# Kernel optimization log

Hardware: AMD Instinct MI355X
Metric: run time of the kernel (lower is better)

The kernel has to match this reference:

```python
import jax, jax.numpy as jnp
import numpy as np

_SQRT1_2 = 0.7071067811865476

B, S, D, N, NCH = 4, 2048, 1024, 32768, 8


def setup_inputs() -> dict:
    key = jax.random.key(0)
    ks = jax.random.split(key, 6)
    return {
        "x": jax.random.normal(ks[0], (B, S, D), jnp.float32),
        "h": jax.random.normal(ks[1], (B, S, D), jnp.float32),
        "emb": jax.random.normal(ks[2], (N, D), jnp.float32),
        "tau_offset": jax.random.normal(ks[3], (B, S, 1), jnp.float32),
        "w_read": jax.random.normal(ks[4], (N, D), jnp.float32),
        "w_write": jax.random.normal(ks[5], (N, D), jnp.float32),
        "n_chunks": NCH,
    }


def _srw_chunked(x, h, emb_unit, tau_offset, w_read, w_write, n_chunks):
    b, s, d = x.shape
    n = emb_unit.shape[0]
    cs = n // n_chunks
    h_bf = h.astype(jnp.bfloat16)
    x_bf = x.astype(jnp.bfloat16)
    emb_bf = emb_unit.astype(jnp.bfloat16)
    read_bf = w_read.astype(jnp.bfloat16)
    write_bf = w_write.astype(jnp.bfloat16)
    z1 = jnp.zeros((b, s, 1), jnp.float32)

    # ---- pass 1: online score statistics over chunks of N ----
    @jax.checkpoint
    def stats_step(carry, i):
        s_sum, sq_sum, cube_sum, ns_sum, ns_sq = carry
        ec = jax.lax.dynamic_slice_in_dim(emb_bf, i * cs, cs, axis=0)
        sc = (h_bf @ ec.T).astype(jnp.float32)  # [B,S,cs]
        s_sum = s_sum + sc.sum(-1, keepdims=True)
        sq_sum = sq_sum + (sc ** 2).sum(-1, keepdims=True)
        cube_sum = cube_sum + (sc ** 3).sum(-1, keepdims=True)
        pns = sc.mean(axis=(0, 1))  # per-neuron mean score [cs]
        return ((s_sum, sq_sum, cube_sum, ns_sum + pns.sum(), ns_sq + (pns ** 2).sum()), None)

    (s_sum, sq_sum, cube_sum, ns_sum, ns_sq), _ = jax.lax.scan(
        stats_step, (z1, z1, z1, jnp.float32(0.0), jnp.float32(0.0)), jnp.arange(n_chunks))

    s_mean = s_sum / n
    s_std = jnp.sqrt(sq_sum / n - s_mean ** 2) + 1e-08
    tau = s_mean + tau_offset * s_std
    cube_mean = cube_sum / n
    central_third = cube_mean - 3.0 * s_mean * s_std ** 2 - s_mean ** 3
    score_skew = jax.lax.stop_gradient((central_third / (s_std ** 3 + 1e-08)).mean())
    mean_score = ns_sum / n
    var_score = ns_sq / n - mean_score ** 2
    score_lb = var_score / (mean_score ** 2 + var_score + 0.01)

    # ---- pass 2: erf-threshold gate + read/write GEMM accumulate ----
    @jax.checkpoint
    def gate_step(carry, i):
        out, wcost, gmax, act, strong, phib, zsum, z075c, z030c, glg = carry
        s0 = i * cs
        ec = jax.lax.dynamic_slice_in_dim(emb_bf, s0, cs, axis=0)
        rc = jax.lax.dynamic_slice_in_dim(read_bf, s0, cs, axis=0)
        wc = jax.lax.dynamic_slice_in_dim(write_bf, s0, cs, axis=0)
        rc = rc / (jnp.linalg.norm(rc, axis=-1, keepdims=True) + 1e-08)
        wc = wc / (jnp.linalg.norm(wc, axis=-1, keepdims=True) + 1e-08)
        z = ((h_bf @ ec.T).astype(jnp.float32) - tau) / s_std  # [B,S,cs]
        phi = 0.5 * (1.0 + jax.lax.erf(z * _SQRT1_2))
        gate = jnp.where(z > 0, z * phi, 0.0)
        xr = x_bf @ rc.T  # [B,S,cs]
        c_out = ((gate.astype(jnp.bfloat16) * xr) @ wc).astype(jnp.float32)  # [B,S,D]
        g_safe = gate + 1e-08
        new = (
            out + c_out,
            wcost + gate.sum(-1, keepdims=True),
            jnp.maximum(gmax, gate.max(-1, keepdims=True)),
            act + (gate > 0.0).astype(jnp.float32).sum(-1, keepdims=True),
            strong + (gate > 0.5).astype(jnp.float32).sum(-1, keepdims=True),
            phib + ((phi > 0.95) | (phi < 0.05)).astype(jnp.float32).sum(-1, keepdims=True),
            zsum + jnp.where(z > 0, z, 0.0).sum(-1, keepdims=True),
            z075c + ((z > 0) & (z < 0.75)).astype(jnp.float32).sum(-1, keepdims=True),
            z030c + ((z > 0) & (z < 0.3)).astype(jnp.float32).sum(-1, keepdims=True),
            glg + (gate * jnp.log(g_safe)).sum(-1, keepdims=True),
        )
        return (new, None)

    init = (jnp.zeros((b, s, d), jnp.float32), z1, jnp.full((b, s, 1), -1e9, jnp.float32),
            z1, z1, z1, z1, z1, z1, z1)
    (raw_out, wcost, gmax, act, strong, phib, zsum, z075c, z030c, glg), _ = jax.lax.scan(
        gate_step, init, jnp.arange(n_chunks))

    den = jnp.maximum(wcost, 1.0)
    out = (raw_out / den).astype(jnp.bfloat16)
    score_std_out = s_std.mean()
    es_out = wcost.mean()
    active_n_mean = act.mean()
    z_mean_active = zsum / (act + 1e-08)
    active_eps = act + 1e-08
    z_lt_075_frac = jax.lax.stop_gradient((z075c / active_eps).mean())
    z_lt_030_frac = jax.lax.stop_gradient((z030c / active_eps).mean())
    tau_abs_mean = jax.lax.stop_gradient(tau).mean()
    active_per_token_std = jax.lax.stop_gradient(act).std()
    gate_sum_eps = wcost + 1e-08
    entropy_per_token = -glg / gate_sum_eps + jnp.log(gate_sum_eps)
    gate_entropy = jax.lax.stop_gradient(entropy_per_token).mean()
    return (out.astype(jnp.float32), act / n, gmax, score_lb, score_std_out, es_out,
            active_n_mean, strong / n, phib / n, z_mean_active, tau_abs_mean,
            z_lt_075_frac, z_lt_030_frac, score_skew, active_per_token_std, gate_entropy)


def reference(x, h, emb, tau_offset, w_read, w_write, n_chunks):
    emb_unit = emb / (jnp.linalg.norm(emb, axis=-1, keepdims=True) + 1e-08)
    return _srw_chunked(x, h, emb_unit, tau_offset, w_read, w_write, n_chunks)
```

## Files before the change

kernel.cpp:

```cpp
#include <hip/hip_runtime.h>

#define DEV __device__ __forceinline__

typedef __attribute__((ext_vector_type(4))) float f32x4;
typedef __attribute__((ext_vector_type(8))) short s16x8;
typedef __attribute__((ext_vector_type(8))) unsigned short u16x8;

static const int NTOK = 8192;
static const int DD   = 1024;
static const int NNEU = 32768;
static const int NC   = 8192;
static const int NREP = 8;

static const int OUT_ACT    = 8388608;
static const int OUT_GMAX   = 8396800;
static const int OUT_SLB    = 8404992;
static const int OUT_SSTD   = 8404993;
static const int OUT_ES     = 8404994;
static const int OUT_ANM    = 8404995;
static const int OUT_STRONG = 8404996;
static const int OUT_PHIB   = 8413188;
static const int OUT_ZMEAN  = 8421380;
static const int OUT_TAUM   = 8429572;
static const int OUT_Z75    = 8429573;
static const int OUT_Z30    = 8429574;
static const int OUT_SKEW   = 8429575;
static const int OUT_ASTD   = 8429576;
static const int OUT_ENT    = 8429577;

DEV unsigned short f2bf(float f){
  unsigned u = __float_as_uint(f);
  u += 0x7fffu + ((u >> 16) & 1u);
  return (unsigned short)(u >> 16);
}
DEV float bf2f(unsigned short h){ return __uint_as_float(((unsigned)h) << 16); }
DEV float rnd_bf(float f){ return bf2f(f2bf(f)); }

template<int AUX>
DEV void gl_lds16(const void* g, void* l){
  __builtin_amdgcn_global_load_lds(
      (const __attribute__((address_space(1))) unsigned int*)g,
      (__attribute__((address_space(3))) unsigned int*)l, 16, 0, AUX);
}

DEV f32x4 mfma16(s16x8 a, s16x8 b, f32x4 c){
  return __builtin_amdgcn_mfma_f32_16x16x32_bf16(a, b, c, 0, 0, 0);
}

template<int AUX>
DEV void stage4(const unsigned short* __restrict__ G, size_t ld, int k0,
                unsigned short* L, int t){
  #pragma unroll
  for (int i = 0; i < 4; i++){
    int ch = i*256 + t;
    int row = ch >> 3, c = ch & 7;
    int cs = c ^ (row & 7);
    int wb = (i*256 + (t & 192)) * 16;
    gl_lds16<AUX>(G + (size_t)row * ld + k0 + cs*8, (char*)L + wb);
  }
}

DEV void stageS(const unsigned short* __restrict__ S0, size_t ldS,
                unsigned short* L, int t){
  #pragma unroll
  for (int i = 0; i < 8; i++){
    int ch = i*256 + t;
    int row = ch >> 4, c = ch & 15;
    int cs = c ^ (row & 15);
    int wb = (i*256 + (t & 192)) * 16;
    gl_lds16<0>(S0 + (size_t)row * ldS + cs*8, (char*)L + wb);
  }
}

DEV s16x8 frg(const unsigned short* L, int R, int kk, int lq){
  int cc = ((kk >> 3) + lq) ^ (R & 7);
  return *(const s16x8*)((const char*)L + R*128 + cc*16);
}

DEV void waitv_bar(){
  asm volatile("s_waitcnt vmcnt(0)" ::: "memory");
  __builtin_amdgcn_s_barrier();
  __builtin_amdgcn_sched_barrier(0);
}

DEV int2 xcd64(){
  int orig = blockIdx.y * 64 + blockIdx.x;
  int xcd = orig & 7, p = orig >> 3;
  int sqy = p >> 6, off = p & 63;
  int2 r;
  r.x = xcd*8 + (off & 7);
  r.y = sqy*8 + (off >> 3);
  return r;
}


template<int RND, int PNS>
__global__ __launch_bounds__(256) void k_rncast(const float* __restrict__ in,
    unsigned short* __restrict__ o, const float* __restrict__ hs,
    float* __restrict__ ns){
  __shared__ float hsh[1024];
  __shared__ float pr[8];
  int t = threadIdx.x, l = t & 63, wv = t >> 6;
  if (PNS){
    for (int i = t; i < 1024; i += 256) hsh[i] = hs[i];
    __syncthreads();
  }
  int row = blockIdx.x * 4 + wv;
  const float4* rp = (const float4*)(in + (size_t)row * DD);
  float4 v[4];
  float ss = 0.f;
  #pragma unroll
  for (int j = 0; j < 4; j++){
    float4 a = rp[j*64 + l];
    if (RND){ a.x = rnd_bf(a.x); a.y = rnd_bf(a.y); a.z = rnd_bf(a.z); a.w = rnd_bf(a.w); }
    v[j] = a;
    ss += a.x*a.x + a.y*a.y + a.z*a.z + a.w*a.w;
  }
  #pragma unroll
  for (int d = 1; d < 64; d <<= 1) ss += __shfl_xor(ss, d);
  float inv = 1.f / (sqrtf(ss) + 1e-8f);
  float dot = 0.f;
  ushort4* op = (ushort4*)(o + (size_t)row * DD);
  #pragma unroll
  for (int j = 0; j < 4; j++){
    ushort4 r;
    r.x = f2bf(v[j].x * inv); r.y = f2bf(v[j].y * inv);
    r.z = f2bf(v[j].z * inv); r.w = f2bf(v[j].w * inv);
    op[j*64 + l] = r;
    if (PNS){
      int c0 = (j*64 + l)*4;
      dot += hsh[c0]*bf2f(r.x) + hsh[c0+1]*bf2f(r.y)
           + hsh[c0+2]*bf2f(r.z) + hsh[c0+3]*bf2f(r.w);
    }
  }
  if (PNS){
    #pragma unroll
    for (int d = 1; d < 64; d <<= 1) dot += __shfl_xor(dot, d);
    if (l == 0){
      float pns = dot * (1.f / 8192.f);
      pr[wv*2] = pns; pr[wv*2 + 1] = pns*pns;
    }
    __syncthreads();
    if (t == 0){
      atomicAdd(ns + 0, pr[0] + pr[2] + pr[4] + pr[6]);
      atomicAdd(ns + 1, pr[1] + pr[3] + pr[5] + pr[7]);
    }
  }
}

__global__ __launch_bounds__(256) void k_wnorm(const float* __restrict__ w_,
                                               float* __restrict__ inv_w){
  int t = threadIdx.x, l = t & 63, wv = t >> 6;
  int row = blockIdx.x * 4 + wv;
  const float4* wp = (const float4*)(w_ + (size_t)row * DD);
  float sw = 0.f;
  #pragma unroll
  for (int j = 0; j < 4; j++){
    float4 c = wp[j*64 + l];
    float c0 = rnd_bf(c.x), c1 = rnd_bf(c.y), c2 = rnd_bf(c.z), c3 = rnd_bf(c.w);
    sw += c0*c0 + c1*c1 + c2*c2 + c3*c3;
  }
  #pragma unroll
  for (int d = 1; d < 64; d <<= 1) sw += __shfl_xor(sw, d);
  if (l == 0) inv_w[row] = 1.f / (sqrtf(sw) + 1e-8f);
}

__global__ __launch_bounds__(256) void k_cast(const float* __restrict__ in,
                                              unsigned short* __restrict__ o){
  size_t i = (size_t)blockIdx.x * 256 + threadIdx.x;
  float4 v = ((const float4*)in)[i];
  ushort4 r;
  r.x = f2bf(v.x); r.y = f2bf(v.y); r.z = f2bf(v.z); r.w = f2bf(v.w);
  ((ushort4*)o)[i] = r;
}

__global__ __launch_bounds__(256) void k_wcnT(const float* __restrict__ w_,
    const float* __restrict__ invw, unsigned short* __restrict__ o){
  __shared__ unsigned short tile[64][65];
  int t = threadIdx.x;
  int n0b = blockIdx.x * 64, d0 = blockIdx.y * 64;
  #pragma unroll
  for (int i = 0; i < 16; i++){
    int idx = t + i*256;
    int r = idx >> 6, c = idx & 63;
    float v = w_[(size_t)(n0b + r) * DD + d0 + c];
    tile[c][r] = f2bf(rnd_bf(v) * invw[n0b + r]);
  }
  __syncthreads();
  #pragma unroll
  for (int i = 0; i < 16; i++){
    int idx = t + i*256;
    int rd = idx >> 6, cn = idx & 63;
    o[(size_t)(d0 + rd) * NNEU + n0b + cn] = tile[rd][cn];
  }
}

__global__ __launch_bounds__(256) void k_hsum(const unsigned short* __restrict__ hb,
                                              float* __restrict__ hs){
  int t = threadIdx.x; int r0 = blockIdx.x * 128;
  float s[4] = {0.f, 0.f, 0.f, 0.f};
  for (int r = 0; r < 128; r++){
    const unsigned short* row = hb + (size_t)(r0 + r) * DD;
    #pragma unroll
    for (int j = 0; j < 4; j++) s[j] += bf2f(row[j*256 + t]);
  }
  #pragma unroll
  for (int j = 0; j < 4; j++) atomicAdd(hs + j*256 + t, s[j]);
}


template<bool DO_STATS>
__global__ __launch_bounds__(256, 2) void k_score(
    const unsigned short* __restrict__ A, const unsigned short* __restrict__ Bm,
    float* __restrict__ s_sum, float* __restrict__ sq_sum, float* __restrict__ cu_sum,
    unsigned short* __restrict__ Sout, int do_store)
{
  __shared__ unsigned short lds[32768];
  const int t = threadIdx.x, l = t & 63, wv = t >> 6;
  const int wm = wv >> 1, wn = wv & 1;
  const int lq = l >> 4, lr = l & 15;
  int2 rm = xcd64();
  const int bx = rm.x, by = rm.y;
  const unsigned short* Ab = A  + (size_t)by * 128 * DD;
  const unsigned short* Bb = Bm + (size_t)bx * 128 * DD;
  f32x4 acc[4][4];
  #pragma unroll
  for (int m = 0; m < 4; m++)
    #pragma unroll
    for (int n = 0; n < 4; n++) acc[m][n] = (f32x4){0.f, 0.f, 0.f, 0.f};

  stage4<0>(Ab, DD, 0, lds, t);
  stage4<0>(Bb, DD, 0, lds + 8192, t);
  waitv_bar();
  int cur = 0;
  for (int ks = 0; ks < 16; ++ks){
    unsigned short* Lc = lds + cur*16384;
    if (ks + 1 < 16){
      unsigned short* Ln = lds + (cur^1)*16384;
      int k0 = (ks+1)*64;
      stage4<0>(Ab, DD, k0, Ln, t);
      stage4<0>(Bb, DD, k0, Ln + 8192, t);
    }
    #pragma unroll
    for (int kk = 0; kk < 64; kk += 32){
      s16x8 af[4], bf4[4];
      #pragma unroll
      for (int m = 0; m < 4; m++) af[m]  = frg(Lc, wm*64 + m*16 + lr, kk, lq);
      #pragma unroll
      for (int n = 0; n < 4; n++) bf4[n] = frg(Lc + 8192, wn*64 + n*16 + lr, kk, lq);
      #pragma unroll
      for (int m = 0; m < 4; m++)
        #pragma unroll
        for (int n = 0; n < 4; n++)
          acc[m][n] = mfma16(af[m], bf4[n], acc[m][n]);
    }
    waitv_bar();
    cur ^= 1;
  }

  unsigned short* sl = lds;
  #pragma unroll
  for (int m = 0; m < 4; m++)
  #pragma unroll
  for (int n = 0; n < 4; n++)
  #pragma unroll
  for (int r = 0; r < 4; r++){
    int rl = wm*64 + m*16 + lq*4 + r;
    int cl = wn*64 + n*16 + lr;
    sl[rl*136 + cl] = f2bf(acc[m][n][r]);
  }
  __syncthreads();

  int row = t >> 1, half = t & 1;
  const unsigned short* sp = &sl[row*136 + half*64];
  unsigned short* Sdst = Sout + (size_t)(by*128 + row) * NC + bx*128 + half*64;
  float s1 = 0.f, s2 = 0.f, s3 = 0.f;
  #pragma unroll
  for (int j = 0; j < 8; j++){
    u16x8 v = *(const u16x8*)(sp + j*8);
    if (do_store) *(u16x8*)(Sdst + j*8) = v;
    if (DO_STATS){
      #pragma unroll
      for (int e = 0; e < 8; e++){
        float f = bf2f(v[e]);
        s1 += f; float f2 = f*f; s2 += f2; s3 += f2*f;
      }
    }
  }
  if (DO_STATS){
    s1 += __shfl_xor(s1, 1); s2 += __shfl_xor(s2, 1); s3 += __shfl_xor(s3, 1);
    if (half == 0){
      int gr = by*128 + row;
      int rep = (bx & 7) * NTOK;
      atomicAdd(s_sum + rep + gr, s1);
      atomicAdd(sq_sum + rep + gr, s2);
      atomicAdd(cu_sum + rep + gr, s3);
    }
  }
}

__global__ __launch_bounds__(256) void k_tau(const float* __restrict__ s_sum,
    const float* __restrict__ sq_sum, const float* __restrict__ tof,
    float* __restrict__ tau, float* __restrict__ rstd){
  int i = blockIdx.x * 256 + threadIdx.x;
  float ssum = 0.f, sqsum = 0.f;
  #pragma unroll
  for (int k = 0; k < NREP; k++){
    ssum  += s_sum[k*NTOK + i];
    sqsum += sq_sum[k*NTOK + i];
  }
  float mean = ssum * (1.f / 32768.f);
  float var  = sqsum * (1.f / 32768.f) - mean*mean;
  float sstd = sqrtf(fmaxf(var, 0.f)) + 1e-8f;
  tau[i]  = mean + tof[i] * sstd;
  rstd[i] = 1.f / sstd;
}


__global__ __launch_bounds__(256, 2) void k_gateS(
    const unsigned short* __restrict__ Xb, const unsigned short* __restrict__ Rb,
    const float* __restrict__ tau, const float* __restrict__ rstd,
    unsigned short* __restrict__ SP, int n0,
    float* __restrict__ wcostp, float* __restrict__ gmaxp, float* __restrict__ actp,
    float* __restrict__ strongp, float* __restrict__ phibp, float* __restrict__ zsump,
    float* __restrict__ z075p, float* __restrict__ z030p, float* __restrict__ glgp)
{
  __shared__ unsigned short lds[32768];
  const int t = threadIdx.x, l = t & 63, wv = t >> 6;
  const int wm = wv >> 1, wn = wv & 1;
  const int lq = l >> 4, lr = l & 15;
  int2 rm = xcd64();
  const int bx = rm.x, by = rm.y;
  const unsigned short* Xp = Xb + (size_t)by * 128 * DD;
  const unsigned short* Rp = Rb + (size_t)(n0 + bx*128) * DD;
  const unsigned short* Stile = SP + (size_t)(by*128) * NC + bx*128;
  f32x4 accX[4][4];
  #pragma unroll
  for (int m = 0; m < 4; m++)
    #pragma unroll
    for (int n = 0; n < 4; n++) accX[m][n] = (f32x4){0.f,0.f,0.f,0.f};

  stage4<0>(Xp, DD, 0, lds, t);
  stage4<0>(Rp, DD, 0, lds + 8192, t);
  waitv_bar();
  int cur = 0;
  for (int ks = 0; ks < 16; ++ks){
    unsigned short* Lc = lds + cur*16384;
    if (ks + 1 < 16){
      unsigned short* Ln = lds + (cur^1)*16384;
      int k0 = (ks+1)*64;
      stage4<0>(Xp, DD, k0, Ln, t);
      stage4<0>(Rp, DD, k0, Ln + 8192, t);
    } else {
      stageS(Stile, NC, lds, t);
    }
    #pragma unroll
    for (int kk = 0; kk < 64; kk += 32){
      s16x8 af[4], bf4[4];
      #pragma unroll
      for (int m = 0; m < 4; m++) af[m]  = frg(Lc, wm*64 + m*16 + lr, kk, lq);
      #pragma unroll
      for (int n = 0; n < 4; n++) bf4[n] = frg(Lc + 8192, wn*64 + n*16 + lr, kk, lq);
      #pragma unroll
      for (int m = 0; m < 4; m++)
        #pragma unroll
        for (int n = 0; n < 4; n++)
          accX[m][n] = mfma16(af[m], bf4[n], accX[m][n]);
    }
    waitv_bar();
    cur ^= 1;
  }
  unsigned short* xrl = lds + 16384;
  #pragma unroll
  for (int m = 0; m < 4; m++)
  #pragma unroll
  for (int n = 0; n < 4; n++)
  #pragma unroll
  for (int r = 0; r < 4; r++){
    int rl = wm*64 + m*16 + lq*4 + r;
    int cl = wn*64 + n*16 + lr;
    int cs = (cl >> 3) ^ (rl & 15);
    xrl[rl*128 + cs*8 + (cl & 7)] = f2bf(accX[m][n][r]);
  }
  __syncthreads();

  int row = t >> 1, half = t & 1;
  int gr = by*128 + row;
  float tauv = tau[gr], rs = rstd[gr];
  unsigned short* Prow = SP + (size_t)gr * NC + bx*128 + half*64;
  float wsum = 0.f, gmx = 0.f, ac = 0.f, stc = 0.f, pb = 0.f;
  float zs = 0.f, z7 = 0.f, z3 = 0.f, gl = 0.f;
  #pragma unroll
  for (int jj = 0; jj < 8; jj++){
    int g  = half*8 + jj;
    int cs = g ^ (row & 15);
    u16x8 s8 = *(const u16x8*)&lds[row*128 + cs*8];
    u16x8 x8 = *(const u16x8*)&lds[16384 + row*128 + cs*8];
    u16x8 pv;
    #pragma unroll
    for (int e = 0; e < 8; e++){
      float sc = bf2f(s8[e]);
      float xr = bf2f(x8[e]);
      float z = (sc - tauv) * rs;
      float phi = 0.5f * (1.0f + erff(z * 0.70710678118654752440f));
      float gate = (z > 0.f) ? z * phi : 0.f;
      wsum += gate; gmx = fmaxf(gmx, gate);
      if (gate > 0.5f) stc += 1.f;
      if (fabsf(z) > 1.6448536f) pb += 1.f;
      if (z > 0.f){ ac += 1.f; zs += z; if (z < 0.75f) z7 += 1.f; if (z < 0.3f) z3 += 1.f; }
      gl += gate * __logf(gate + 1e-8f);
      pv[e] = f2bf(rnd_bf(gate) * xr);
    }
    *(u16x8*)(Prow + jj*8) = pv;
  }
  wsum += __shfl_xor(wsum, 1); gmx = fmaxf(gmx, __shfl_xor(gmx, 1));
  ac   += __shfl_xor(ac, 1);   stc += __shfl_xor(stc, 1);
  pb   += __shfl_xor(pb, 1);   zs  += __shfl_xor(zs, 1);
  z7   += __shfl_xor(z7, 1);   z3  += __shfl_xor(z3, 1);
  gl   += __shfl_xor(gl, 1);
  if (half == 0){
    int rep = (bx & 7) * NTOK;
    atomicAdd(wcostp + rep + gr, wsum);
    atomicMax((int*)(gmaxp + rep + gr), __float_as_int(gmx));
    atomicAdd(actp + rep + gr, ac);
    atomicAdd(strongp + rep + gr, stc);
    atomicAdd(phibp + rep + gr, pb);
    atomicAdd(zsump + rep + gr, zs);
    atomicAdd(z075p + rep + gr, z7);
    atomicAdd(z030p + rep + gr, z3);
    atomicAdd(glgp + rep + gr, gl);
  }
}

__global__ __launch_bounds__(256) void k_redw(const float* __restrict__ wcostp,
                                              float* __restrict__ wc){
  int i = blockIdx.x * 256 + threadIdx.x;
  float s = 0.f;
  #pragma unroll
  for (int k = 0; k < NREP; k++) s += wcostp[k*NTOK + i];
  wc[i] = s;
}


__global__ __launch_bounds__(256, 2) void k_out_gemm(
    const unsigned short* __restrict__ Pm, const unsigned short* __restrict__ Bt,
    float* __restrict__ outp, const float* __restrict__ wcost, int accum, int fin)
{
  __shared__ unsigned short lds[32768];
  const int t = threadIdx.x, l = t & 63, wv = t >> 6;
  const int wm = wv >> 1, wn = wv & 1;
  const int lq = l >> 4, lr = l & 15;
  const int bx = blockIdx.x, by = blockIdx.y;
  const unsigned short* Ab = Pm + (size_t)by * 128 * NC;
  const unsigned short* Bb = Bt + (size_t)bx * 128 * NNEU;
  f32x4 acc[4][4];
  #pragma unroll
  for (int m = 0; m < 4; m++)
    #pragma unroll
    for (int n = 0; n < 4; n++) acc[m][n] = (f32x4){0.f,0.f,0.f,0.f};

  const int NT = NC / 64;
  stage4<2>(Ab, NC, 0, lds, t);
  stage4<0>(Bb, NNEU, 0, lds + 8192, t);
  waitv_bar();
  int cur = 0;
  for (int ks = 0; ks < NT; ++ks){
    unsigned short* Lc = lds + cur*16384;
    if (ks + 1 < NT){
      unsigned short* Ln = lds + (cur^1)*16384;
      int k0 = (ks+1)*64;
      stage4<2>(Ab, NC, k0, Ln, t);
      stage4<0>(Bb, NNEU, k0, Ln + 8192, t);
    }
    #pragma unroll
    for (int kk = 0; kk < 64; kk += 32){
      s16x8 af[4], bf4[4];
      #pragma unroll
      for (int m = 0; m < 4; m++) af[m]  = frg(Lc, wm*64 + m*16 + lr, kk, lq);
      #pragma unroll
      for (int n = 0; n < 4; n++) bf4[n] = frg(Lc + 8192, wn*64 + n*16 + lr, kk, lq);
      #pragma unroll
      for (int m = 0; m < 4; m++)
        #pragma unroll
        for (int n = 0; n < 4; n++)
          acc[m][n] = mfma16(af[m], bf4[n], acc[m][n]);
    }
    waitv_bar();
    cur ^= 1;
  }
  #pragma unroll
  for (int m = 0; m < 4; m++)
  #pragma unroll
  for (int r = 0; r < 4; r++){
    int gr = by*128 + wm*64 + m*16 + lq*4 + r;
    float den = fin ? fmaxf(wcost[gr], 1.f) : 1.f;
    #pragma unroll
    for (int n = 0; n < 4; n++){
      int dc = bx*128 + wn*64 + n*16 + lr;
      float* o = outp + (size_t)gr * DD + dc;
      float v = acc[m][n][r];
      if (accum) v += *o;
      if (fin)   v = rnd_bf(v / den);
      *o = v;
    }
  }
}


__global__ __launch_bounds__(1024) void k_final(
    const float* __restrict__ s_sum, const float* __restrict__ sq_sum,
    const float* __restrict__ cu_sum, const float* __restrict__ tof,
    const float* __restrict__ wcostp, const float* __restrict__ gmaxp,
    const float* __restrict__ actp, const float* __restrict__ strongp,
    const float* __restrict__ phibp, const float* __restrict__ zsump,
    const float* __restrict__ z075p, const float* __restrict__ z030p,
    const float* __restrict__ glgp, const float* __restrict__ ns,
    float* __restrict__ out)
{
  int tid = threadIdx.x;
  float s0=0,s1=0,s2=0,s3=0,s4=0,s5=0,s6=0,s7=0,s8=0;
  for (int i = tid; i < NTOK; i += 1024){
    float ssum=0, sqsum=0, cusum=0, wc=0, gmax=0, ac=0, stc=0, pb=0, zsv=0, z7=0, z3=0, glv=0;
    #pragma unroll
    for (int k = 0; k < NREP; k++){
      int o = k*NTOK + i;
      ssum += s_sum[o]; sqsum += sq_sum[o]; cusum += cu_sum[o];
      wc += wcostp[o]; gmax = fmaxf(gmax, gmaxp[o]);
      ac += actp[o]; stc += strongp[o]; pb += phibp[o];
      zsv += zsump[o]; z7 += z075p[o]; z3 += z030p[o]; glv += glgp[o];
    }
    float mean = ssum * (1.f / 32768.f);
    float var  = sqsum * (1.f / 32768.f) - mean*mean;
    float sstd = sqrtf(fmaxf(var, 0.f)) + 1e-8f;
    float tauv = mean + tof[i] * sstd;
    out[OUT_ACT + i]    = ac * (1.f / 32768.f);
    out[OUT_GMAX + i]   = gmax;
    out[OUT_STRONG + i] = stc * (1.f / 32768.f);
    out[OUT_PHIB + i]   = pb * (1.f / 32768.f);
    out[OUT_ZMEAN + i]  = zsv / (ac + 1e-8f);
    float c3 = cusum * (1.f / 32768.f) - 3.f*mean*sstd*sstd - mean*mean*mean;
    float skew = c3 / (sstd*sstd*sstd + 1e-8f);
    float gse = wc + 1e-8f;
    float ent = -glv / gse + logf(gse);
    s0 += sstd; s1 += wc; s2 += ac; s3 += ac*ac; s4 += tauv;
    s5 += z7 / (ac + 1e-8f); s6 += z3 / (ac + 1e-8f); s7 += skew; s8 += ent;
  }
  __shared__ float rb[16][9];
  int lane = tid & 63, wid = tid >> 6;
  #pragma unroll
  for (int d = 1; d < 64; d <<= 1){
    s0 += __shfl_xor(s0,d); s1 += __shfl_xor(s1,d); s2 += __shfl_xor(s2,d);
    s3 += __shfl_xor(s3,d); s4 += __shfl_xor(s4,d); s5 += __shfl_xor(s5,d);
    s6 += __shfl_xor(s6,d); s7 += __shfl_xor(s7,d); s8 += __shfl_xor(s8,d);
  }
  if (lane == 0){
    rb[wid][0]=s0; rb[wid][1]=s1; rb[wid][2]=s2; rb[wid][3]=s3; rb[wid][4]=s4;
    rb[wid][5]=s5; rb[wid][6]=s6; rb[wid][7]=s7; rb[wid][8]=s8;
  }
  __syncthreads();
  if (tid == 0){
    float S[9];
    for (int k = 0; k < 9; k++){ float a = 0.f; for (int w2 = 0; w2 < 16; w2++) a += rb[w2][k]; S[k] = a; }
    const float inv = 1.f / 8192.f;
    float act_mean = S[2] * inv;
    out[OUT_SSTD] = S[0] * inv;
    out[OUT_ES]   = S[1] * inv;
    out[OUT_ANM]  = act_mean;
    out[OUT_ASTD] = sqrtf(fmaxf(S[3]*inv - act_mean*act_mean, 0.f));
    out[OUT_TAUM] = S[4] * inv;
    out[OUT_Z75]  = S[5] * inv;
    out[OUT_Z30]  = S[6] * inv;
    out[OUT_SKEW] = S[7] * inv;
    out[OUT_ENT]  = S[8] * inv;
    float ms = ns[0] * (1.f / 32768.f);
    float vs = ns[1] * (1.f / 32768.f) - ms*ms;
    out[OUT_SLB] = vs / (ms*ms + vs + 0.01f);
  }
}


extern "C" void kernel_launch(void* const* d_in, const int* in_sizes, int n_in,
                              void* d_out, int out_size, void* d_ws, size_t ws_size,
                              hipStream_t stream)
{
  (void)in_sizes; (void)n_in; (void)out_size;
  const float* x   = (const float*)d_in[0];
  const float* h   = (const float*)d_in[1];
  const float* emb = (const float*)d_in[2];
  const float* tof = (const float*)d_in[3];
  const float* wr  = (const float*)d_in[4];
  const float* ww  = (const float*)d_in[5];
  float* out = (float*)d_out;
  char* ws = (char*)d_ws;

  size_t off = 0;
  auto get = [&](size_t n){ size_t o = off; off += (n + 255) & ~(size_t)255; return o; };
  unsigned short* rcn_bf = (unsigned short*)(ws + get((size_t)NNEU*DD*2));
  unsigned short* emb_bf = (unsigned short*)(ws + get((size_t)NNEU*DD*2));
  unsigned short* wcnT   = (unsigned short*)(ws + get((size_t)DD*NNEU*2));
  unsigned short* h_bf   = (unsigned short*)(ws + get((size_t)NTOK*DD*2));
  unsigned short* x_bf   = (unsigned short*)(ws + get((size_t)NTOK*DD*2));
  float* inv_w   = (float*)(ws + get(NNEU*4));
  float* tau     = (float*)(ws + get(NTOK*4));
  float* rstd    = (float*)(ws + get(NTOK*4));
  float* wc_comb = (float*)(ws + get(NTOK*4));
  size_t zoff = off;
  float* hsum   = (float*)(ws + get(DD*4));
  float* s_sum  = (float*)(ws + get(NREP*NTOK*4));
  float* sq_sum = (float*)(ws + get(NREP*NTOK*4));
  float* cu_sum = (float*)(ws + get(NREP*NTOK*4));
  float* wcost  = (float*)(ws + get(NREP*NTOK*4));
  float* gmax   = (float*)(ws + get(NREP*NTOK*4));
  float* act    = (float*)(ws + get(NREP*NTOK*4));
  float* strong = (float*)(ws + get(NREP*NTOK*4));
  float* phib   = (float*)(ws + get(NREP*NTOK*4));
  float* zsum   = (float*)(ws + get(NREP*NTOK*4));
  float* z075   = (float*)(ws + get(NREP*NTOK*4));
  float* z030   = (float*)(ws + get(NREP*NTOK*4));
  float* glg    = (float*)(ws + get(NREP*NTOK*4));
  float* ns     = (float*)(ws + get(256));
  size_t zlen = off - zoff;

  const size_t szS = (size_t)NTOK * NC * 2;
  size_t poff = (off + 4095) & ~(size_t)4095;
  size_t avail = ws_size > poff ? ws_size - poff : 0;
  int kst = (int)(avail / szS);
  if (kst > 4) kst = 4;
  if (kst < 1) kst = 1;
  unsigned short* Sb = (unsigned short*)(ws + poff);

  hipMemsetAsync(ws + zoff, 0, zlen, stream);

  dim3 b256(256);
  dim3 gC(64, 64);
  k_cast<<<dim3(NTOK*DD/4/256), b256, 0, stream>>>(h, h_bf);
  k_cast<<<dim3(NTOK*DD/4/256), b256, 0, stream>>>(x, x_bf);
  k_hsum<<<dim3(NTOK/128), b256, 0, stream>>>(h_bf, hsum);
  k_rncast<0,1><<<dim3(NNEU/4), b256, 0, stream>>>(emb, emb_bf, hsum, ns);
  k_rncast<1,0><<<dim3(NNEU/4), b256, 0, stream>>>(wr, rcn_bf, nullptr, nullptr);
  k_wnorm<<<dim3(NNEU/4), b256, 0, stream>>>(ww, inv_w);

  for (int c = 0; c < 4; ++c){
    unsigned short* slot = Sb + (size_t)(c < kst ? c : 0) * NTOK * NC;
    k_score<true><<<gC, b256, 0, stream>>>(h_bf, emb_bf + (size_t)c*NC*DD,
        s_sum, sq_sum, cu_sum, slot, c < kst ? 1 : 0);
  }
  k_tau<<<dim3(NTOK/256), b256, 0, stream>>>(s_sum, sq_sum, tof, tau, rstd);
  k_wcnT<<<dim3(NNEU/64, DD/64), b256, 0, stream>>>(ww, inv_w, wcnT);

  for (int c = 0; c < 4; ++c){
    int slot_i = (c < kst) ? c : (c % kst);
    unsigned short* slot = Sb + (size_t)slot_i * NTOK * NC;
    if (c >= kst){
      k_score<false><<<gC, b256, 0, stream>>>(h_bf, emb_bf + (size_t)c*NC*DD,
          nullptr, nullptr, nullptr, slot, 1);
    }
    k_gateS<<<gC, b256, 0, stream>>>(x_bf, rcn_bf, tau, rstd, slot, c*NC,
        wcost, gmax, act, strong, phib, zsum, z075, z030, glg);
    if (c == 3) k_redw<<<dim3(NTOK/256), b256, 0, stream>>>(wcost, wc_comb);
    k_out_gemm<<<dim3(DD/128, NTOK/128), b256, 0, stream>>>(slot, wcnT + (size_t)c*NC,
        out, wc_comb, c > 0 ? 1 : 0, c == 3 ? 1 : 0);
  }
  k_final<<<dim3(1), dim3(1024), 0, stream>>>(s_sum, sq_sum, cu_sum, tof, wcost, gmax,
      act, strong, phib, zsum, z075, z030, glg, ns, out);
}
```

Baseline: 3.907 ms.

## Enlarge score and gate GEMM tiles to 256x256 with a 4-stage pipeline

The score and gate GEMM kernels move from 128x128 tiles with 256 threads and double-buffered BK=64 staging to 256x256 tiles with 512 threads. Staging becomes a 4-deep ring of BK=32 buffers with counted vmcnt waits, and s_setprio wraps the MFMA bursts. The gate kernel now reads the stored score tile straight from global memory into registers instead of staging it through LDS. The aim is more reuse per loaded byte and better latency hiding. The cost is 128KB of LDS per block, which likely allows only one block per CU, plus higher register pressure.

```diff
diff --git a/kernel.cpp b/kernel.cpp
--- a/kernel.cpp
+++ b/kernel.cpp
@@ -59,37 +59,41 @@
     gl_lds16<AUX>(G + (size_t)row * ld + k0 + cs*8, (char*)L + wb);
   }
 }
-
-DEV void stageS(const unsigned short* __restrict__ S0, size_t ldS,
-                unsigned short* L, int t){
-  #pragma unroll
-  for (int i = 0; i < 8; i++){
-    int ch = i*256 + t;
-    int row = ch >> 4, c = ch & 15;
-    int cs = c ^ (row & 15);
-    int wb = (i*256 + (t & 192)) * 16;
-    gl_lds16<0>(S0 + (size_t)row * ldS + cs*8, (char*)L + wb);
-  }
-}
-
 DEV s16x8 frg(const unsigned short* L, int R, int kk, int lq){
   int cc = ((kk >> 3) + lq) ^ (R & 7);
   return *(const s16x8*)((const char*)L + R*128 + cc*16);
 }
-
 DEV void waitv_bar(){
   asm volatile("s_waitcnt vmcnt(0)" ::: "memory");
   __builtin_amdgcn_s_barrier();
   __builtin_amdgcn_sched_barrier(0);
 }
 
-DEV int2 xcd64(){
-  int orig = blockIdx.y * 64 + blockIdx.x;
+DEV void stageK(const unsigned short* __restrict__ GA,
+                const unsigned short* __restrict__ GB,
+                int kt, unsigned short* Lb, int t){
+  #pragma unroll
+  for (int i = 0; i < 2; i++){
+    int ch = i*512 + t, row = ch >> 2, c = ch & 3;
+    gl_lds16<0>(GA + (size_t)row * DD + kt*32 + (c ^ (row & 3))*8,
+                (char*)Lb + (i*512 + (t & 448))*16);
+  }
+  #pragma unroll
+  for (int i = 0; i < 2; i++){
+    int ch = i*512 + t, row = ch >> 2, c = ch & 3;
+    gl_lds16<0>(GB + (size_t)row * DD + kt*32 + (c ^ (row & 3))*8,
+                (char*)Lb + 16384 + (i*512 + (t & 448))*16);
+  }
+}
+DEV s16x8 frg32(const unsigned short* L, int R, int lq){
+  int cs = lq ^ (R & 3);
+  return *(const s16x8*)(L + R*32 + cs*8);
+}
+
+DEV int2 xcd32(){
+  int orig = blockIdx.y * 32 + blockIdx.x;
   int xcd = orig & 7, p = orig >> 3;
-  int sqy = p >> 6, off = p & 63;
-  int2 r;
-  r.x = xcd*8 + (off & 7);
-  r.y = sqy*8 + (off >> 3);
+  int2 r; r.x = xcd*4 + (p & 3); r.y = p >> 2;
   return r;
 }
 
@@ -209,75 +213,85 @@
 }
 
 
+#define CORE_LOOP(GA, GB)                                                     \
+  stageK(GA, GB, 0, lds + 0*16384, t);                                        \
+  stageK(GA, GB, 1, lds + 1*16384, t);                                        \
+  stageK(GA, GB, 2, lds + 2*16384, t);                                        \
+  _Pragma("unroll 1")                                                         \
+  for (int ks = 0; ks < 32; ++ks){                                            \
+    if (ks < 30)       asm volatile("s_waitcnt vmcnt(8)" ::: "memory");       \
+    else if (ks == 30) asm volatile("s_waitcnt vmcnt(4)" ::: "memory");       \
+    else               asm volatile("s_waitcnt vmcnt(0)" ::: "memory");       \
+    __builtin_amdgcn_s_barrier();                                             \
+    __builtin_amdgcn_sched_barrier(0);                                        \
+    if (ks + 3 < 32) stageK(GA, GB, ks + 3, lds + ((ks+3)&3)*16384, t);       \
+    const unsigned short* lA = lds + (ks&3)*16384;                            \
+    const unsigned short* lB = lA + 8192;                                     \
+    s16x8 af[8], b0, b1;                                                      \
+    _Pragma("unroll")                                                         \
+    for (int m = 0; m < 8; m++) af[m] = frg32(lA, wm*128 + m*16 + lr, lq);    \
+    b0 = frg32(lB, wn*64 +  0 + lr, lq);                                      \
+    b1 = frg32(lB, wn*64 + 16 + lr, lq);                                      \
+    __builtin_amdgcn_s_setprio(1);                                            \
+    _Pragma("unroll")                                                         \
+    for (int m = 0; m < 8; m++) acc[m][0] = mfma16(af[m], b0, acc[m][0]);     \
+    _Pragma("unroll")                                                         \
+    for (int m = 0; m < 8; m++) acc[m][1] = mfma16(af[m], b1, acc[m][1]);     \
+    __builtin_amdgcn_s_setprio(0);                                            \
+    b0 = frg32(lB, wn*64 + 32 + lr, lq);                                      \
+    b1 = frg32(lB, wn*64 + 48 + lr, lq);                                      \
+    __builtin_amdgcn_s_setprio(1);                                            \
+    _Pragma("unroll")                                                         \
+    for (int m = 0; m < 8; m++) acc[m][2] = mfma16(af[m], b0, acc[m][2]);     \
+    _Pragma("unroll")                                                         \
+    for (int m = 0; m < 8; m++) acc[m][3] = mfma16(af[m], b1, acc[m][3]);     \
+    __builtin_amdgcn_s_setprio(0);                                            \
+  }                                                                           \
+  __syncthreads();
+
+
 template<bool DO_STATS>
-__global__ __launch_bounds__(256, 2) void k_score(
+__global__ __launch_bounds__(512, 2) void k_score(
     const unsigned short* __restrict__ A, const unsigned short* __restrict__ Bm,
     float* __restrict__ s_sum, float* __restrict__ sq_sum, float* __restrict__ cu_sum,
     unsigned short* __restrict__ Sout, int do_store)
 {
-  __shared__ unsigned short lds[32768];
+  __shared__ unsigned short lds[65536];
   const int t = threadIdx.x, l = t & 63, wv = t >> 6;
-  const int wm = wv >> 1, wn = wv & 1;
+  const int wm = wv >> 2, wn = wv & 3;
   const int lq = l >> 4, lr = l & 15;
-  int2 rm = xcd64();
+  int2 rm = xcd32();
   const int bx = rm.x, by = rm.y;
-  const unsigned short* Ab = A  + (size_t)by * 128 * DD;
-  const unsigned short* Bb = Bm + (size_t)bx * 128 * DD;
-  f32x4 acc[4][4];
-  #pragma unroll
-  for (int m = 0; m < 4; m++)
+  const unsigned short* Ab = A  + (size_t)by * 256 * DD;
+  const unsigned short* Bb = Bm + (size_t)bx * 256 * DD;
+  f32x4 acc[8][4];
+  #pragma unroll
+  for (int m = 0; m < 8; m++)
     #pragma unroll
     for (int n = 0; n < 4; n++) acc[m][n] = (f32x4){0.f, 0.f, 0.f, 0.f};
 
-  stage4<0>(Ab, DD, 0, lds, t);
-  stage4<0>(Bb, DD, 0, lds + 8192, t);
-  waitv_bar();
-  int cur = 0;
-  for (int ks = 0; ks < 16; ++ks){
-    unsigned short* Lc = lds + cur*16384;
-    if (ks + 1 < 16){
-      unsigned short* Ln = lds + (cur^1)*16384;
-      int k0 = (ks+1)*64;
-      stage4<0>(Ab, DD, k0, Ln, t);
-      stage4<0>(Bb, DD, k0, Ln + 8192, t);
-    }
-    #pragma unroll
-    for (int kk = 0; kk < 64; kk += 32){
-      s16x8 af[4], bf4[4];
-      #pragma unroll
-      for (int m = 0; m < 4; m++) af[m]  = frg(Lc, wm*64 + m*16 + lr, kk, lq);
-      #pragma unroll
-      for (int n = 0; n < 4; n++) bf4[n] = frg(Lc + 8192, wn*64 + n*16 + lr, kk, lq);
-      #pragma unroll
-      for (int m = 0; m < 4; m++)
-        #pragma unroll
-        for (int n = 0; n < 4; n++)
-          acc[m][n] = mfma16(af[m], bf4[n], acc[m][n]);
-    }
-    waitv_bar();
-    cur ^= 1;
-  }
-
-  unsigned short* sl = lds;
-  #pragma unroll
-  for (int m = 0; m < 4; m++)
+  CORE_LOOP(Ab, Bb)
+
+  #pragma unroll
+  for (int m = 0; m < 8; m++)
   #pragma unroll
   for (int n = 0; n < 4; n++)
   #pragma unroll
   for (int r = 0; r < 4; r++){
-    int rl = wm*64 + m*16 + lq*4 + r;
-    int cl = wn*64 + n*16 + lr;
-    sl[rl*136 + cl] = f2bf(acc[m][n][r]);
+    int row = wm*128 + m*16 + lq*4 + r;
+    int cl  = wn*64 + n*16 + lr;
+    int cs  = (cl >> 3) ^ (row & 31);
+    lds[row*256 + cs*8 + (cl & 7)] = f2bf(acc[m][n][r]);
   }
   __syncthreads();
 
   int row = t >> 1, half = t & 1;
-  const unsigned short* sp = &sl[row*136 + half*64];
-  unsigned short* Sdst = Sout + (size_t)(by*128 + row) * NC + bx*128 + half*64;
+  unsigned short* Sdst = Sout + (size_t)(by*256 + row) * NC + bx*256 + half*128;
   float s1 = 0.f, s2 = 0.f, s3 = 0.f;
   #pragma unroll
-  for (int j = 0; j < 8; j++){
-    u16x8 v = *(const u16x8*)(sp + j*8);
+  for (int j = 0; j < 16; j++){
+    int cs = (half*16 + j) ^ (row & 31);
+    u16x8 v = *(const u16x8*)&lds[row*256 + cs*8];
     if (do_store) *(u16x8*)(Sdst + j*8) = v;
     if (DO_STATS){
       #pragma unroll
@@ -290,7 +304,7 @@
   if (DO_STATS){
     s1 += __shfl_xor(s1, 1); s2 += __shfl_xor(s2, 1); s3 += __shfl_xor(s3, 1);
     if (half == 0){
-      int gr = by*128 + row;
+      int gr = by*256 + row;
       int rep = (bx & 7) * NTOK;
       atomicAdd(s_sum + rep + gr, s1);
       atomicAdd(sq_sum + rep + gr, s2);
@@ -317,7 +331,7 @@
 }
 
 
-__global__ __launch_bounds__(256, 2) void k_gateS(
+__global__ __launch_bounds__(512, 2) void k_gateS(
     const unsigned short* __restrict__ Xb, const unsigned short* __restrict__ Rb,
     const float* __restrict__ tau, const float* __restrict__ rstd,
     unsigned short* __restrict__ SP, int n0,
@@ -325,77 +339,50 @@
     float* __restrict__ strongp, float* __restrict__ phibp, float* __restrict__ zsump,
     float* __restrict__ z075p, float* __restrict__ z030p, float* __restrict__ glgp)
 {
-  __shared__ unsigned short lds[32768];
+  __shared__ unsigned short lds[65536];
   const int t = threadIdx.x, l = t & 63, wv = t >> 6;
-  const int wm = wv >> 1, wn = wv & 1;
+  const int wm = wv >> 2, wn = wv & 3;
   const int lq = l >> 4, lr = l & 15;
-  int2 rm = xcd64();
+  int2 rm = xcd32();
   const int bx = rm.x, by = rm.y;
-  const unsigned short* Xp = Xb + (size_t)by * 128 * DD;
-  const unsigned short* Rp = Rb + (size_t)(n0 + bx*128) * DD;
-  const unsigned short* Stile = SP + (size_t)(by*128) * NC + bx*128;
-  f32x4 accX[4][4];
-  #pragma unroll
-  for (int m = 0; m < 4; m++)
-    #pragma unroll
-    for (int n = 0; n < 4; n++) accX[m][n] = (f32x4){0.f,0.f,0.f,0.f};
-
-  stage4<0>(Xp, DD, 0, lds, t);
-  stage4<0>(Rp, DD, 0, lds + 8192, t);
-  waitv_bar();
-  int cur = 0;
-  for (int ks = 0; ks < 16; ++ks){
-    unsigned short* Lc = lds + cur*16384;
-    if (ks + 1 < 16){
-      unsigned short* Ln = lds + (cur^1)*16384;
-      int k0 = (ks+1)*64;
-      stage4<0>(Xp, DD, k0, Ln, t);
-      stage4<0>(Rp, DD, k0, Ln + 8192, t);
-    } else {
-      stageS(Stile, NC, lds, t);
-    }
-    #pragma unroll
-    for (int kk = 0; kk < 64; kk += 32){
-      s16x8 af[4], bf4[4];
-      #pragma unroll
-      for (int m = 0; m < 4; m++) af[m]  = frg(Lc, wm*64 + m*16 + lr, kk, lq);
-      #pragma unroll
-      for (int n = 0; n < 4; n++) bf4[n] = frg(Lc + 8192, wn*64 + n*16 + lr, kk, lq);
-      #pragma unroll
-      for (int m = 0; m < 4; m++)
-        #pragma unroll
-        for (int n = 0; n < 4; n++)
-          accX[m][n] = mfma16(af[m], bf4[n], accX[m][n]);
-    }
-    waitv_bar();
-    cur ^= 1;
-  }
-  unsigned short* xrl = lds + 16384;
-  #pragma unroll
-  for (int m = 0; m < 4; m++)
+  const unsigned short* Xp = Xb + (size_t)by * 256 * DD;
+  const unsigned short* Rp = Rb + (size_t)(n0 + bx*256) * DD;
+  f32x4 acc[8][4];
+  #pragma unroll
+  for (int m = 0; m < 8; m++)
+    #pragma unroll
+    for (int n = 0; n < 4; n++) acc[m][n] = (f32x4){0.f,0.f,0.f,0.f};
+
+  CORE_LOOP(Xp, Rp)
+
+  int row = t >> 1, half = t & 1;
+  int gr = by*256 + row;
+  unsigned short* Srow = SP + (size_t)gr * NC + bx*256 + half*128;
+  u16x8 sv[16];
+  #pragma unroll
+  for (int j = 0; j < 16; j++) sv[j] = *(const u16x8*)(Srow + j*8);
+
+  #pragma unroll
+  for (int m = 0; m < 8; m++)
   #pragma unroll
   for (int n = 0; n < 4; n++)
   #pragma unroll
   for (int r = 0; r < 4; r++){
-    int rl = wm*64 + m*16 + lq*4 + r;
+    int rw = wm*128 + m*16 + lq*4 + r;
     int cl = wn*64 + n*16 + lr;
-    int cs = (cl >> 3) ^ (rl & 15);
-    xrl[rl*128 + cs*8 + (cl & 7)] = f2bf(accX[m][n][r]);
+    int cs = (cl >> 3) ^ (rw & 31);
+    lds[rw*256 + cs*8 + (cl & 7)] = f2bf(acc[m][n][r]);
   }
   __syncthreads();
 
-  int row = t >> 1, half = t & 1;
-  int gr = by*128 + row;
   float tauv = tau[gr], rs = rstd[gr];
-  unsigned short* Prow = SP + (size_t)gr * NC + bx*128 + half*64;
   float wsum = 0.f, gmx = 0.f, ac = 0.f, stc = 0.f, pb = 0.f;
   float zs = 0.f, z7 = 0.f, z3 = 0.f, gl = 0.f;
   #pragma unroll
-  for (int jj = 0; jj < 8; jj++){
-    int g  = half*8 + jj;
-    int cs = g ^ (row & 15);
-    u16x8 s8 = *(const u16x8*)&lds[row*128 + cs*8];
-    u16x8 x8 = *(const u16x8*)&lds[16384 + row*128 + cs*8];
+  for (int j = 0; j < 16; j++){
+    int cs = (half*16 + j) ^ (row & 31);
+    u16x8 x8 = *(const u16x8*)&lds[row*256 + cs*8];
+    u16x8 s8 = sv[j];
     u16x8 pv;
     #pragma unroll
     for (int e = 0; e < 8; e++){
@@ -411,7 +398,7 @@
       gl += gate * __logf(gate + 1e-8f);
       pv[e] = f2bf(rnd_bf(gate) * xr);
     }
-    *(u16x8*)(Prow + jj*8) = pv;
+    *(u16x8*)(Srow + j*8) = pv;
   }
   wsum += __shfl_xor(wsum, 1); gmx = fmaxf(gmx, __shfl_xor(gmx, 1));
   ac   += __shfl_xor(ac, 1);   stc += __shfl_xor(stc, 1);
@@ -631,8 +618,8 @@
 
   hipMemsetAsync(ws + zoff, 0, zlen, stream);
 
-  dim3 b256(256);
-  dim3 gC(64, 64);
+  dim3 b256(256), b512(512);
+  dim3 gC(32, 32);
   k_cast<<<dim3(NTOK*DD/4/256), b256, 0, stream>>>(h, h_bf);
   k_cast<<<dim3(NTOK*DD/4/256), b256, 0, stream>>>(x, x_bf);
   k_hsum<<<dim3(NTOK/128), b256, 0, stream>>>(h_bf, hsum);
@@ -642,7 +629,7 @@
 
   for (int c = 0; c < 4; ++c){
     unsigned short* slot = Sb + (size_t)(c < kst ? c : 0) * NTOK * NC;
-    k_score<true><<<gC, b256, 0, stream>>>(h_bf, emb_bf + (size_t)c*NC*DD,
+    k_score<true><<<gC, b512, 0, stream>>>(h_bf, emb_bf + (size_t)c*NC*DD,
         s_sum, sq_sum, cu_sum, slot, c < kst ? 1 : 0);
   }
   k_tau<<<dim3(NTOK/256), b256, 0, stream>>>(s_sum, sq_sum, tof, tau, rstd);
@@ -652,10 +639,10 @@
     int slot_i = (c < kst) ? c : (c % kst);
     unsigned short* slot = Sb + (size_t)slot_i * NTOK * NC;
     if (c >= kst){
-      k_score<false><<<gC, b256, 0, stream>>>(h_bf, emb_bf + (size_t)c*NC*DD,
+      k_score<false><<<gC, b512, 0, stream>>>(h_bf, emb_bf + (size_t)c*NC*DD,
           nullptr, nullptr, nullptr, slot, 1);
     }
-    k_gateS<<<gC, b256, 0, stream>>>(x_bf, rcn_bf, tau, rstd, slot, c*NC,
+    k_gateS<<<gC, b512, 0, stream>>>(x_bf, rcn_bf, tau, rstd, slot, c*NC,
         wcost, gmax, act, strong, phib, zsum, z075, z030, glg);
     if (c == 3) k_redw<<<dim3(NTOK/256), b256, 0, stream>>>(wcost, wc_comb);
     k_out_gemm<<<dim3(DD/128, NTOK/128), b256, 0, stream>>>(slot, wcnT + (size_t)c*NC,
```

Result: slower. 4.329 ms (+10.8%).

## Fuse score recomputation GEMM into gate kernel for non-stored chunks

Applied to the files above, without the earlier changes.

For chunks whose scores were not kept from the stats pass, a new dual-GEMM kernel computes both the h·emb score tile and the x·w_read tile in one kernel, then applies the shared gate epilogue. This replaces a separate score kernel plus a gate kernel, which wrote the bf16 score tile to global memory and read it back. The fused kernel stages four operand tiles per k-step with no double buffering and keeps two accumulator sets, which raises register pressure and may lower occupancy or overlap.

```diff
diff --git a/kernel.cpp b/kernel.cpp
--- a/kernel.cpp
+++ b/kernel.cpp
@@ -314,6 +314,59 @@
   float sstd = sqrtf(fmaxf(var, 0.f)) + 1e-8f;
   tau[i]  = mean + tof[i] * sstd;
   rstd[i] = 1.f / sstd;
+}
+
+DEV void gate_epilogue(unsigned short* lds, unsigned short* SP,
+    const float* tau, const float* rstd, int bx, int by, int t,
+    float* wcostp, float* gmaxp, float* actp, float* strongp, float* phibp,
+    float* zsump, float* z075p, float* z030p, float* glgp)
+{
+  int row = t >> 1, half = t & 1;
+  int gr = by*128 + row;
+  float tauv = tau[gr], rs = rstd[gr];
+  unsigned short* Prow = SP + (size_t)gr * NC + bx*128 + half*64;
+  float wsum = 0.f, gmx = 0.f, ac = 0.f, stc = 0.f, pb = 0.f;
+  float zs = 0.f, z7 = 0.f, z3 = 0.f, gl = 0.f;
+  #pragma unroll
+  for (int jj = 0; jj < 8; jj++){
+    int g  = half*8 + jj;
+    int cs = g ^ (row & 15);
+    u16x8 s8 = *(const u16x8*)&lds[row*128 + cs*8];
+    u16x8 x8 = *(const u16x8*)&lds[16384 + row*128 + cs*8];
+    u16x8 pv;
+    #pragma unroll
+    for (int e = 0; e < 8; e++){
+      float sc = bf2f(s8[e]);
+      float xr = bf2f(x8[e]);
+      float z = (sc - tauv) * rs;
+      float phi = 0.5f * (1.0f + erff(z * 0.70710678118654752440f));
+      float gate = (z > 0.f) ? z * phi : 0.f;
+      wsum += gate; gmx = fmaxf(gmx, gate);
+      if (gate > 0.5f) stc += 1.f;
+      if (fabsf(z) > 1.6448536f) pb += 1.f;
+      if (z > 0.f){ ac += 1.f; zs += z; if (z < 0.75f) z7 += 1.f; if (z < 0.3f) z3 += 1.f; }
+      gl += gate * __logf(gate + 1e-8f);
+      pv[e] = f2bf(rnd_bf(gate) * xr);
+    }
+    *(u16x8*)(Prow + jj*8) = pv;
+  }
+  wsum += __shfl_xor(wsum, 1); gmx = fmaxf(gmx, __shfl_xor(gmx, 1));
+  ac   += __shfl_xor(ac, 1);   stc += __shfl_xor(stc, 1);
+  pb   += __shfl_xor(pb, 1);   zs  += __shfl_xor(zs, 1);
+  z7   += __shfl_xor(z7, 1);   z3  += __shfl_xor(z3, 1);
+  gl   += __shfl_xor(gl, 1);
+  if (half == 0){
+    int rep = (bx & 7) * NTOK;
+    atomicAdd(wcostp + rep + gr, wsum);
+    atomicMax((int*)(gmaxp + rep + gr), __float_as_int(gmx));
+    atomicAdd(actp + rep + gr, ac);
+    atomicAdd(strongp + rep + gr, stc);
+    atomicAdd(phibp + rep + gr, pb);
+    atomicAdd(zsump + rep + gr, zs);
+    atomicAdd(z075p + rep + gr, z7);
+    atomicAdd(z030p + rep + gr, z3);
+    atomicAdd(glgp + rep + gr, gl);
+  }
 }
 
 
@@ -384,52 +437,87 @@
   }
   __syncthreads();
 
-  int row = t >> 1, half = t & 1;
-  int gr = by*128 + row;
-  float tauv = tau[gr], rs = rstd[gr];
-  unsigned short* Prow = SP + (size_t)gr * NC + bx*128 + half*64;
-  float wsum = 0.f, gmx = 0.f, ac = 0.f, stc = 0.f, pb = 0.f;
-  float zs = 0.f, z7 = 0.f, z3 = 0.f, gl = 0.f;
-  #pragma unroll
-  for (int jj = 0; jj < 8; jj++){
-    int g  = half*8 + jj;
-    int cs = g ^ (row & 15);
-    u16x8 s8 = *(const u16x8*)&lds[row*128 + cs*8];
-    u16x8 x8 = *(const u16x8*)&lds[16384 + row*128 + cs*8];
-    u16x8 pv;
-    #pragma unroll
-    for (int e = 0; e < 8; e++){
-      float sc = bf2f(s8[e]);
-      float xr = bf2f(x8[e]);
-      float z = (sc - tauv) * rs;
-      float phi = 0.5f * (1.0f + erff(z * 0.70710678118654752440f));
-      float gate = (z > 0.f) ? z * phi : 0.f;
-      wsum += gate; gmx = fmaxf(gmx, gate);
-      if (gate > 0.5f) stc += 1.f;
-      if (fabsf(z) > 1.6448536f) pb += 1.f;
-      if (z > 0.f){ ac += 1.f; zs += z; if (z < 0.75f) z7 += 1.f; if (z < 0.3f) z3 += 1.f; }
-      gl += gate * __logf(gate + 1e-8f);
-      pv[e] = f2bf(rnd_bf(gate) * xr);
-    }
-    *(u16x8*)(Prow + jj*8) = pv;
-  }
-  wsum += __shfl_xor(wsum, 1); gmx = fmaxf(gmx, __shfl_xor(gmx, 1));
-  ac   += __shfl_xor(ac, 1);   stc += __shfl_xor(stc, 1);
-  pb   += __shfl_xor(pb, 1);   zs  += __shfl_xor(zs, 1);
-  z7   += __shfl_xor(z7, 1);   z3  += __shfl_xor(z3, 1);
-  gl   += __shfl_xor(gl, 1);
-  if (half == 0){
-    int rep = (bx & 7) * NTOK;
-    atomicAdd(wcostp + rep + gr, wsum);
-    atomicMax((int*)(gmaxp + rep + gr), __float_as_int(gmx));
-    atomicAdd(actp + rep + gr, ac);
-    atomicAdd(strongp + rep + gr, stc);
-    atomicAdd(phibp + rep + gr, pb);
-    atomicAdd(zsump + rep + gr, zs);
-    atomicAdd(z075p + rep + gr, z7);
-    atomicAdd(z030p + rep + gr, z3);
-    atomicAdd(glgp + rep + gr, gl);
-  }
+  gate_epilogue(lds, SP, tau, rstd, bx, by, t,
+      wcostp, gmaxp, actp, strongp, phibp, zsump, z075p, z030p, glgp);
+}
+
+
+__global__ __launch_bounds__(256, 2) void k_gate_dual(
+    const unsigned short* __restrict__ Hb, const unsigned short* __restrict__ Ec,
+    const unsigned short* __restrict__ Xb, const unsigned short* __restrict__ Rc,
+    const float* __restrict__ tau, const float* __restrict__ rstd,
+    unsigned short* __restrict__ SP,
+    float* __restrict__ wcostp, float* __restrict__ gmaxp, float* __restrict__ actp,
+    float* __restrict__ strongp, float* __restrict__ phibp, float* __restrict__ zsump,
+    float* __restrict__ z075p, float* __restrict__ z030p, float* __restrict__ glgp)
+{
+  __shared__ unsigned short lds[32768];
+  const int t = threadIdx.x, l = t & 63, wv = t >> 6;
+  const int wm = wv >> 1, wn = wv & 1;
+  const int lq = l >> 4, lr = l & 15;
+  int2 rm = xcd64();
+  const int bx = rm.x, by = rm.y;
+  const unsigned short* Hp = Hb + (size_t)by * 128 * DD;
+  const unsigned short* Xp = Xb + (size_t)by * 128 * DD;
+  const unsigned short* Ep = Ec + (size_t)(bx*128) * DD;
+  const unsigned short* Rp = Rc + (size_t)(bx*128) * DD;
+  f32x4 accS[4][4], accX[4][4];
+  #pragma unroll
+  for (int m = 0; m < 4; m++)
+    #pragma unroll
+    for (int n = 0; n < 4; n++){
+      accS[m][n] = (f32x4){0.f,0.f,0.f,0.f};
+      accX[m][n] = (f32x4){0.f,0.f,0.f,0.f};
+    }
+
+  for (int k0 = 0; k0 < DD; k0 += 64){
+    __syncthreads();
+    stage4<0>(Hp, DD, k0, lds +     0, t);
+    stage4<0>(Ep, DD, k0, lds +  8192, t);
+    stage4<0>(Xp, DD, k0, lds + 16384, t);
+    stage4<0>(Rp, DD, k0, lds + 24576, t);
+    asm volatile("s_waitcnt vmcnt(0)" ::: "memory");
+    __syncthreads();
+    #pragma unroll
+    for (int kk = 0; kk < 64; kk += 32){
+      s16x8 af[4], bf4[4];
+      #pragma unroll
+      for (int m = 0; m < 4; m++) af[m]  = frg(lds, wm*64 + m*16 + lr, kk, lq);
+      #pragma unroll
+      for (int n = 0; n < 4; n++) bf4[n] = frg(lds + 8192, wn*64 + n*16 + lr, kk, lq);
+      #pragma unroll
+      for (int m = 0; m < 4; m++)
+        #pragma unroll
+        for (int n = 0; n < 4; n++)
+          accS[m][n] = mfma16(af[m], bf4[n], accS[m][n]);
+      #pragma unroll
+      for (int m = 0; m < 4; m++) af[m]  = frg(lds + 16384, wm*64 + m*16 + lr, kk, lq);
+      #pragma unroll
+      for (int n = 0; n < 4; n++) bf4[n] = frg(lds + 24576, wn*64 + n*16 + lr, kk, lq);
+      #pragma unroll
+      for (int m = 0; m < 4; m++)
+        #pragma unroll
+        for (int n = 0; n < 4; n++)
+          accX[m][n] = mfma16(af[m], bf4[n], accX[m][n]);
+    }
+  }
+  __syncthreads();
+  #pragma unroll
+  for (int m = 0; m < 4; m++)
+  #pragma unroll
+  for (int n = 0; n < 4; n++)
+  #pragma unroll
+  for (int r = 0; r < 4; r++){
+    int rl = wm*64 + m*16 + lq*4 + r;
+    int cl = wn*64 + n*16 + lr;
+    int cs = (cl >> 3) ^ (rl & 15);
+    lds[rl*128 + cs*8 + (cl & 7)]         = f2bf(accS[m][n][r]);
+    lds[16384 + rl*128 + cs*8 + (cl & 7)] = f2bf(accX[m][n][r]);
+  }
+  __syncthreads();
+
+  gate_epilogue(lds, SP, tau, rstd, bx, by, t,
+      wcostp, gmaxp, actp, strongp, phibp, zsump, z075p, z030p, glgp);
 }
 
 __global__ __launch_bounds__(256) void k_redw(const float* __restrict__ wcostp,
@@ -651,12 +739,14 @@
   for (int c = 0; c < 4; ++c){
     int slot_i = (c < kst) ? c : (c % kst);
     unsigned short* slot = Sb + (size_t)slot_i * NTOK * NC;
-    if (c >= kst){
-      k_score<false><<<gC, b256, 0, stream>>>(h_bf, emb_bf + (size_t)c*NC*DD,
-          nullptr, nullptr, nullptr, slot, 1);
-    }
-    k_gateS<<<gC, b256, 0, stream>>>(x_bf, rcn_bf, tau, rstd, slot, c*NC,
-        wcost, gmax, act, strong, phib, zsum, z075, z030, glg);
+    if (c < kst){
+      k_gateS<<<gC, b256, 0, stream>>>(x_bf, rcn_bf, tau, rstd, slot, c*NC,
+          wcost, gmax, act, strong, phib, zsum, z075, z030, glg);
+    } else {
+      k_gate_dual<<<gC, b256, 0, stream>>>(h_bf, emb_bf + (size_t)c*NC*DD,
+          x_bf, rcn_bf + (size_t)c*NC*DD, tau, rstd, slot,
+          wcost, gmax, act, strong, phib, zsum, z075, z030, glg);
+    }
     if (c == 3) k_redw<<<dim3(NTOK/256), b256, 0, stream>>>(wcost, wc_comb);
     k_out_gemm<<<dim3(DD/128, NTOK/128), b256, 0, stream>>>(slot, wcnT + (size_t)c*NC,
         out, wc_comb, c > 0 ? 1 : 0, c == 3 ? 1 : 0);
```

Result: faster. 3.776 ms (-3.3%).
